# Kernel optimization log

Measured on AMD Instinct MI355X. Metric: run time of the kernel, lower is better.

Reference implementation:

```python
import jax, jax.numpy as jnp
import numpy as np

B, N, COUT, CIN, H, W = 16, 4, 256, 256, 64, 64


def setup_inputs() -> dict:
    key = jax.random.key(0)
    k1, k2, k3, k4 = jax.random.split(key, 4)
    x = jax.random.normal(k1, (B, CIN, H, W), jnp.float32)
    alphas = jax.random.uniform(k2, (B, N), jnp.float32)          # routing weights (lambdas)
    angles = jax.random.normal(k3, (B, N), jnp.float32) * 0.5     # thetas, mixed signs
    # kaiming_normal_(mode='fan_out', relu): std = sqrt(2 / (Cout * k * k))
    std = np.sqrt(2.0 / (COUT * 9)).astype(np.float32)
    weight = jax.random.normal(k4, (N, COUT, CIN, 3, 3), jnp.float32) * std
    return {"x": x, "alphas": alphas, "angles": angles, "weight": weight}


def _rot_mats(thetas):
    """thetas: [M] -> rotation matrices [M, 9, 9] (row, col), matching torch builder."""
    xc = jnp.cos(thetas)
    ys = jnp.sin(thetas)
    a = xc - ys
    b = xc * ys
    c = xc + ys
    z = jnp.zeros_like(xc)
    o = jnp.ones_like(xc)

    def mat(rows):
        # rows: list of 9 lists of 9 [M]-arrays -> [M, 9, 9]
        return jnp.stack([jnp.stack(r, axis=-1) for r in rows], axis=-2)

    pos = mat([
        [a, 1 - a, z, z, z, z, z, z, z],
        [z, xc - b, b, z, 1 - c + b, ys - b, z, z, z],
        [z, z, a, z, z, 1 - a, z, z, z],
        [b, ys - b, z, xc - b, 1 - c + b, z, z, z, z],
        [z, z, z, z, o, z, z, z, z],
        [z, z, z, z, 1 - c + b, xc - b, z, ys - b, b],
        [z, z, z, 1 - a, z, z, a, z, z],
        [z, z, z, ys - b, 1 - c + b, z, b, xc - b, z],
        [z, z, z, z, z, z, z, 1 - a, a],
    ])
    neg = mat([
        [c, z, z, 1 - c, z, z, z, z, z],
        [-b, xc + b, z, b - ys, 1 - a - b, z, z, z, z],
        [z, 1 - c, c, z, z, z, z, z, z],
        [z, z, z, xc + b, 1 - a - b, z, -b, b - ys, z],
        [z, z, z, z, o, z, z, z, z],
        [z, b - ys, -b, z, 1 - a - b, xc + b, z, z, z],
        [z, z, z, z, z, z, c, 1 - c, z],
        [z, z, z, z, 1 - a - b, b - ys, z, xc + b, -b],
        [z, z, z, z, z, 1 - c, z, z, c],
    ])
    m = (thetas >= 0).astype(thetas.dtype)[:, None, None]
    return m * pos + (1 - m) * neg


def reference(x, alphas, angles, weight):
    bsz, Cin, h, w = x.shape
    n, Cout = weight.shape[0], weight.shape[1]
    # [bsz, n, 9, 9] rotation matrices scaled by routing lambdas
    rm = _rot_mats(angles.reshape(-1)).reshape(bsz, n, 9, 9)
    rm = rm * alphas[:, :, None, None]
    # weights [n, Cout, Cin, 3, 3] -> [n, 9, Cout*Cin]
    Wf = weight.transpose(0, 3, 4, 1, 2).reshape(n, 9, Cout * Cin)
    # mix over kernel_number n and source tap q -> per-sample rotated kernels
    rw = jnp.einsum('bnpq,nqm->bpm', rm, Wf)          # [bsz, 9, Cout*Cin]
    rw = rw.reshape(bsz, 3, 3, Cout, Cin).transpose(0, 3, 4, 1, 2)
    rw = rw.reshape(bsz * Cout, Cin, 3, 3)
    # per-sample conv via grouped conv on flattened batch
    xr = x.reshape(1, bsz * Cin, h, w)
    out = jax.lax.conv_general_dilated(
        xr, rw, window_strides=(1, 1), padding=((1, 1), (1, 1)),
        dimension_numbers=('NCHW', 'OIHW', 'NCHW'), feature_group_count=bsz)
    return out.reshape(bsz, Cout, out.shape[2], out.shape[3])
```

## Files before the change

### kernel.cpp

```cpp
#include <hip/hip_runtime.h>
#include <hip/hip_bf16.h>

#define B_    16
#define N_    4
#define COUT  256
#define CIN   256
#define H_    64
#define W_    64
#define K_TOT (CIN * 9)
#define HW    (H_ * W_)
#define NKT   72
#define PAD   66
#define PLANE (PAD * PAD)

typedef __attribute__((ext_vector_type(8))) short short8;
typedef __attribute__((ext_vector_type(4))) float f32x4;
typedef unsigned short ushort_t;

static __device__ __forceinline__ ushort_t f2bf(float f) {
    __hip_bfloat16 h = __float2bfloat16(f);
    return *reinterpret_cast<ushort_t*>(&h);
}

typedef __attribute__((address_space(3))) unsigned int lds_u32;
typedef __attribute__((address_space(1))) const unsigned int glb_u32;
static __device__ __forceinline__ void gl_lds16(const ushort_t* g, ushort_t* l) {
    __builtin_amdgcn_global_load_lds((glb_u32*)g, (lds_u32*)l, 16, 0, 0);
}

#define BARRIER() asm volatile("s_barrier" ::: "memory")
#define VMCNTN(N) asm volatile("s_waitcnt vmcnt(" #N ")" ::: "memory")

__global__ void rot_mats_kernel(const float* __restrict__ alphas,
                                const float* __restrict__ angles,
                                float* __restrict__ rm) {
    int i = threadIdx.x;
    if (i >= B_ * N_) return;
    float th = angles[i], al = alphas[i];
    float xc = cosf(th), ys = sinf(th);
    float a = xc - ys, b = xc * ys, c = xc + ys;
    float r[81];
#pragma unroll
    for (int j = 0; j < 81; ++j) r[j] = 0.f;
    if (th >= 0.f) {
        r[0] = a;          r[1] = 1.f - a;
        r[10] = xc - b;    r[11] = b;        r[13] = 1.f - c + b; r[14] = ys - b;
        r[20] = a;         r[23] = 1.f - a;
        r[27] = b;         r[28] = ys - b;   r[30] = xc - b;      r[31] = 1.f - c + b;
        r[40] = 1.f;
        r[49] = 1.f - c + b; r[50] = xc - b; r[52] = ys - b;      r[53] = b;
        r[57] = 1.f - a;   r[60] = a;
        r[66] = ys - b;    r[67] = 1.f - c + b; r[69] = b;        r[70] = xc - b;
        r[79] = 1.f - a;   r[80] = a;
    } else {
        r[0] = c;          r[3] = 1.f - c;
        r[9] = -b;         r[10] = xc + b;   r[12] = b - ys;      r[13] = 1.f - a - b;
        r[19] = 1.f - c;   r[20] = c;
        r[30] = xc + b;    r[31] = 1.f - a - b; r[33] = -b;       r[34] = b - ys;
        r[40] = 1.f;
        r[46] = b - ys;    r[47] = -b;       r[49] = 1.f - a - b; r[50] = xc + b;
        r[60] = c;         r[61] = 1.f - c;
        r[67] = 1.f - a - b; r[68] = b - ys; r[70] = xc + b;      r[71] = -b;
        r[77] = 1.f - c;   r[80] = c;
    }
#pragma unroll
    for (int j = 0; j < 81; ++j) rm[i * 81 + j] = r[j] * al;
}

__global__ __launch_bounds__(256)
void build_rw_kernel(const float* __restrict__ weight,
                     const float* __restrict__ rm,
                     ushort_t* __restrict__ rw) {
    __shared__ float rms[N_ * 81];
    int tid = threadIdx.x;
    int b = blockIdx.y;
    for (int j = tid; j < N_ * 81; j += 256)
        rms[j] = rm[b * N_ * 81 + j];
    __syncthreads();

    int idx = blockIdx.x * 256 + tid;
    int cout = idx >> 8, cin = idx & 255;

    float wv[N_][9];
#pragma unroll
    for (int n = 0; n < N_; ++n)
#pragma unroll
        for (int q = 0; q < 9; ++q)
            wv[n][q] = weight[(size_t)(n * (COUT * CIN) + idx) * 9 + q];

    ushort_t* dst = rw + (size_t)(b * COUT + cout) * K_TOT + cin;
#pragma unroll
    for (int p = 0; p < 9; ++p) {
        float s = 0.f;
#pragma unroll
        for (int n = 0; n < N_; ++n)
#pragma unroll
            for (int q = 0; q < 9; ++q)
                s += rms[n * 81 + p * 9 + q] * wv[n][q];
        dst[p * 256] = f2bf(s);
    }
}

__global__ __launch_bounds__(256)
void halo_zero_kernel(ushort_t* __restrict__ xt) {
    ushort_t* base = xt + (size_t)blockIdx.x * PLANE * 64;
    int t = threadIdx.x;
    for (int i = t; i < 260; i += 256) {
        int py, px;
        if (i < 66)       { py = 0;  px = i; }
        else if (i < 132) { py = 65; px = i - 66; }
        else if (i < 196) { py = i - 132 + 1; px = 0; }
        else              { py = i - 196 + 1; px = 65; }
        ushort_t* d = base + (size_t)(py * PAD + px) * 64;
        int4 z = {0, 0, 0, 0};
#pragma unroll
        for (int q = 0; q < 8; ++q) *(int4*)(d + q * 8) = z;
    }
}

__global__ __launch_bounds__(256)
void nhwc_kernel(const float* __restrict__ x, ushort_t* __restrict__ xt) {
    int y    = blockIdx.x;
    int cb32 = blockIdx.y;
    int b    = blockIdx.z;
    __shared__ ushort_t tileT[64][40];
    int t = threadIdx.x;

    int ci = t & 31, seg = t >> 5;
    const float* src = x + ((size_t)(b * CIN + cb32 * 32 + ci) * HW + y * 64 + seg * 8);
    float4 f0 = ((const float4*)src)[0];
    float4 f1 = ((const float4*)src)[1];
#pragma unroll
    for (int q = 0; q < 4; ++q) tileT[seg * 8 + q][ci]     = f2bf(((float*)&f0)[q]);
#pragma unroll
    for (int q = 0; q < 4; ++q) tileT[seg * 8 + 4 + q][ci] = f2bf(((float*)&f1)[q]);
    __syncthreads();

    int px = t >> 2, cseg = t & 3;
    ushort_t* dst = xt + ((size_t)(b * 4 + (cb32 >> 1)) * PLANE + (y + 1) * PAD + px + 1) * 64
                       + (cb32 & 1) * 32 + cseg * 8;
    *(int4*)dst = *(const int4*)&tileT[px][cseg * 8];
}

__global__ __launch_bounds__(512, 4)
void conv_kernel(const ushort_t* __restrict__ xt,
                 const ushort_t* __restrict__ rw,
                 float* __restrict__ out) {
    int bid0 = blockIdx.x;
    int bid = (bid0 & 7) * 64 + (bid0 >> 3);
    int ch    = bid & 1;
    int ptile = (bid >> 1) & 15;
    int b     = bid >> 5;
    int m0 = ch * 128;
    int y0 = ptile * 4;
    int tid = threadIdx.x;
    int lane = tid & 63, wid = tid >> 6;
    int wm = wid >> 2, wn = wid & 3;
    int rA = lane & 15, kseg = lane >> 4;

    __shared__ __align__(16) ushort_t As[3][4096];
    __shared__ __align__(16) ushort_t Bs[3][8192];
    ushort_t* AsB = &As[0][0];
    ushort_t* BsB = &Bs[0][0];

    f32x4 acc[4][4] = {};

    const ushort_t* rwb = rw + (size_t)(b * COUT + m0) * K_TOT;
    const ushort_t* xtb = xt + ((size_t)b * 4 * PLANE + (size_t)y0 * PAD) * 64;

    {
    }
    int la = tid >> 3, sa = tid & 7;
    int ca = sa ^ (la & 7);
    const ushort_t* aSrc = rwb + (size_t)(2 * la + (ca >> 2)) * K_TOT + (ca & 3) * 8;
    const int aDst = tid * 8;
    int bsrc[2], bDst[2];
#pragma unroll
    for (int i = 0; i < 2; ++i) {
        int u = i * 512 + tid;
        int lb = u >> 3, sb = u & 7;
        int cb = sb ^ (lb & 7);
        int px = 2 * lb + (cb >> 2);
        bsrc[i] = ((px >> 6) * PAD + (px & 63)) * 64 + (cb & 3) * 8;
        bDst[i] = u * 8;
    }
    const int slotR = (kseg + 4 * (rA & 1)) ^ ((rA >> 1) & 7);
    const int aRd = (wm * 32 + (rA >> 1)) * 64 + slotR * 8;
    const int bRd = (wn * 32 + (rA >> 1)) * 64 + slotR * 8;

#define STAGE(KT, Q)                                                           \
    {                                                                          \
        int p_ = (KT) >> 3, sub_ = (KT) & 7;                                   \
        int ph_ = p_ / 3, pw_ = p_ - 3 * ph_;                                  \
        gl_lds16(aSrc + p_ * 256 + sub_ * 32, AsB + (Q) * 4096 + aDst);        \
        const ushort_t* sb_ = xtb + (size_t)((sub_ >> 1) * PLANE + ph_ * PAD + pw_) * 64 \
                              + (sub_ & 1) * 32;                               \
        gl_lds16(sb_ + bsrc[0], BsB + (Q) * 8192 + bDst[0]);                   \
        gl_lds16(sb_ + bsrc[1], BsB + (Q) * 8192 + bDst[1]);                   \
    }

    STAGE(0, 0);
    STAGE(1, 1);
    VMCNTN(3);
    BARRIER();

    int qc = 0;
    for (int kt = 0; kt < NKT; ++kt) {
        int qs = qc + 2; if (qs >= 3) qs -= 3;
        if (kt + 2 < NKT) STAGE(kt + 2, qs);

        short8 af[4], bf[4];
#pragma unroll
        for (int mi = 0; mi < 4; ++mi)
            af[mi] = *(const short8*)(AsB + qc * 4096 + aRd + mi * 512);
#pragma unroll
        for (int ni = 0; ni < 4; ++ni)
            bf[ni] = *(const short8*)(BsB + qc * 8192 + bRd + ni * 512);

        __builtin_amdgcn_s_setprio(1);
#pragma unroll
        for (int mi = 0; mi < 4; ++mi)
#pragma unroll
            for (int ni = 0; ni < 4; ++ni)
                acc[mi][ni] = __builtin_amdgcn_mfma_f32_16x16x32_bf16(
                    af[mi], bf[ni], acc[mi][ni], 0, 0, 0);
        __builtin_amdgcn_s_setprio(0);

        if (kt <= NKT - 3)      { VMCNTN(3); }
        else if (kt == NKT - 2) { VMCNTN(0); }
        BARRIER();
        qc = (qc == 2) ? 0 : qc + 1;
    }
#undef STAGE

    int row0 = (lane >> 4) * 4;
    int col  = lane & 15;
    float* outb = out + ((size_t)(b * COUT) + m0) * HW + ptile * 256;
#pragma unroll
    for (int mi = 0; mi < 4; ++mi)
#pragma unroll
        for (int ni = 0; ni < 4; ++ni)
#pragma unroll
            for (int rr = 0; rr < 4; ++rr) {
                int m = wm * 64 + mi * 16 + row0 + rr;
                int n = wn * 64 + ni * 16 + col;
                outb[(size_t)m * HW + n] = acc[mi][ni][rr];
            }
}

extern "C" void kernel_launch(void* const* d_in, const int* in_sizes, int n_in,
                              void* d_out, int out_size, void* d_ws, size_t ws_size,
                              hipStream_t stream) {
    const float* x      = (const float*)d_in[0];
    const float* alphas = (const float*)d_in[1];
    const float* angles = (const float*)d_in[2];
    const float* weight = (const float*)d_in[3];
    float* out = (float*)d_out;

    ushort_t* rw = (ushort_t*)d_ws;
    ushort_t* xt = (ushort_t*)((char*)d_ws + (size_t)B_ * COUT * K_TOT * 2);
    float*    rm = (float*)((char*)d_ws + (size_t)B_ * COUT * K_TOT * 2
                                        + (size_t)64 * PLANE * 64 * 2);

    rot_mats_kernel<<<1, 64, 0, stream>>>(alphas, angles, rm);
    build_rw_kernel<<<dim3(COUT * CIN / 256, B_), 256, 0, stream>>>(weight, rm, rw);
    halo_zero_kernel<<<64, 256, 0, stream>>>(xt);
    nhwc_kernel<<<dim3(64, 8, B_), 256, 0, stream>>>(x, xt);
    conv_kernel<<<512, 512, 0, stream>>>(xt, rw, out);
}
```

Before: 122.8 us.

## Enlarge conv tile to full 256 output channels with split MFMA phases

Each conv block now computes all 256 output channels for its pixel tile instead of 128. That halves the grid to 256 blocks and lets each block reuse its loaded input tile twice as much. The K-step is split into two MFMA halves, with the A and B global-to-LDS stages interleaved between barriers. Accumulators double to 32 f32x4 per thread and occupancy drops to 2 blocks/SM with more LDS. This risks register pressure, lower parallelism (256 blocks on 256 CUs), and extra barriers.

```diff
diff --git a/kernel.cpp b/kernel.cpp
--- a/kernel.cpp
+++ b/kernel.cpp
@@ -142,109 +142,120 @@
     *(int4*)dst = *(const int4*)&tileT[px][cseg * 8];
 }
 
-__global__ __launch_bounds__(512, 4)
+__global__ __launch_bounds__(512, 2)
 void conv_kernel(const ushort_t* __restrict__ xt,
                  const ushort_t* __restrict__ rw,
                  float* __restrict__ out) {
     int bid0 = blockIdx.x;
-    int bid = (bid0 & 7) * 64 + (bid0 >> 3);
-    int ch    = bid & 1;
-    int ptile = (bid >> 1) & 15;
-    int b     = bid >> 5;
-    int m0 = ch * 128;
+    int bid = (bid0 & 7) * 32 + (bid0 >> 3);
+    int b     = bid >> 4;
+    int ptile = bid & 15;
     int y0 = ptile * 4;
     int tid = threadIdx.x;
     int lane = tid & 63, wid = tid >> 6;
     int wm = wid >> 2, wn = wid & 3;
     int rA = lane & 15, kseg = lane >> 4;
 
-    __shared__ __align__(16) ushort_t As[3][4096];
+    __shared__ __align__(16) ushort_t As[3][8192];
     __shared__ __align__(16) ushort_t Bs[3][8192];
     ushort_t* AsB = &As[0][0];
     ushort_t* BsB = &Bs[0][0];
 
-    f32x4 acc[4][4] = {};
-
-    const ushort_t* rwb = rw + (size_t)(b * COUT + m0) * K_TOT;
+    f32x4 acc[8][4] = {};
+
+    const ushort_t* rwb = rw + (size_t)b * COUT * K_TOT;
     const ushort_t* xtb = xt + ((size_t)b * 4 * PLANE + (size_t)y0 * PAD) * 64;
 
-    {
-    }
-    int la = tid >> 3, sa = tid & 7;
-    int ca = sa ^ (la & 7);
-    const ushort_t* aSrc = rwb + (size_t)(2 * la + (ca >> 2)) * K_TOT + (ca & 3) * 8;
-    const int aDst = tid * 8;
-    int bsrc[2], bDst[2];
+    int asrc[2], bsrc[2], uDst[2];
 #pragma unroll
     for (int i = 0; i < 2; ++i) {
         int u = i * 512 + tid;
-        int lb = u >> 3, sb = u & 7;
-        int cb = sb ^ (lb & 7);
-        int px = 2 * lb + (cb >> 2);
-        bsrc[i] = ((px >> 6) * PAD + (px & 63)) * 64 + (cb & 3) * 8;
-        bDst[i] = u * 8;
+        int l = u >> 3, s = u & 7;
+        int c = s ^ (l & 7);
+        int row = 2 * l + (c >> 2);
+        asrc[i] = row * K_TOT + (c & 3) * 8;
+        bsrc[i] = ((row >> 6) * PAD + (row & 63)) * 64 + (c & 3) * 8;
+        uDst[i] = u * 8;
     }
     const int slotR = (kseg + 4 * (rA & 1)) ^ ((rA >> 1) & 7);
-    const int aRd = (wm * 32 + (rA >> 1)) * 64 + slotR * 8;
+    const int aRd = (wm * 64 + (rA >> 1)) * 64 + slotR * 8;
     const int bRd = (wn * 32 + (rA >> 1)) * 64 + slotR * 8;
 
-#define STAGE(KT, Q)                                                           \
+#define STAGE_A(KT, Q)                                                         \
+    {                                                                          \
+        int p_ = (KT) >> 3, sub_ = (KT) & 7;                                   \
+        int ako = p_ * 256 + sub_ * 32;                                        \
+        gl_lds16(rwb + asrc[0] + ako, AsB + (Q) * 8192 + uDst[0]);             \
+        gl_lds16(rwb + asrc[1] + ako, AsB + (Q) * 8192 + uDst[1]);             \
+    }
+
+#define STAGE_B(KT, Q)                                                         \
     {                                                                          \
         int p_ = (KT) >> 3, sub_ = (KT) & 7;                                   \
         int ph_ = p_ / 3, pw_ = p_ - 3 * ph_;                                  \
-        gl_lds16(aSrc + p_ * 256 + sub_ * 32, AsB + (Q) * 4096 + aDst);        \
         const ushort_t* sb_ = xtb + (size_t)((sub_ >> 1) * PLANE + ph_ * PAD + pw_) * 64 \
                               + (sub_ & 1) * 32;                               \
-        gl_lds16(sb_ + bsrc[0], BsB + (Q) * 8192 + bDst[0]);                   \
-        gl_lds16(sb_ + bsrc[1], BsB + (Q) * 8192 + bDst[1]);                   \
-    }
-
-    STAGE(0, 0);
-    STAGE(1, 1);
-    VMCNTN(3);
+        gl_lds16(sb_ + bsrc[0], BsB + (Q) * 8192 + uDst[0]);                   \
+        gl_lds16(sb_ + bsrc[1], BsB + (Q) * 8192 + uDst[1]);                   \
+    }
+
+#define DO_MFMA(MH)                                                            \
+    __builtin_amdgcn_s_setprio(1);                                             \
+    _Pragma("unroll")                                                          \
+    for (int mi = 0; mi < 4; ++mi)                                             \
+        _Pragma("unroll")                                                      \
+        for (int ni = 0; ni < 4; ++ni)                                         \
+            acc[(MH) * 4 + mi][ni] = __builtin_amdgcn_mfma_f32_16x16x32_bf16(  \
+                af[mi], bf[ni], acc[(MH) * 4 + mi][ni], 0, 0, 0);              \
+    __builtin_amdgcn_s_setprio(0);
+
+    STAGE_A(0, 0); STAGE_B(0, 0);
+    STAGE_A(1, 1); STAGE_B(1, 1);
+    VMCNTN(4);
     BARRIER();
 
+    short8 af[4], bf[4];
     int qc = 0;
     for (int kt = 0; kt < NKT; ++kt) {
         int qs = qc + 2; if (qs >= 3) qs -= 3;
-        if (kt + 2 < NKT) STAGE(kt + 2, qs);
-
-        short8 af[4], bf[4];
+        bool more = (kt + 2 < NKT);
 #pragma unroll
         for (int mi = 0; mi < 4; ++mi)
-            af[mi] = *(const short8*)(AsB + qc * 4096 + aRd + mi * 512);
+            af[mi] = *(const short8*)(AsB + qc * 8192 + aRd + mi * 512);
 #pragma unroll
         for (int ni = 0; ni < 4; ++ni)
             bf[ni] = *(const short8*)(BsB + qc * 8192 + bRd + ni * 512);
-
-        __builtin_amdgcn_s_setprio(1);
+        if (more) STAGE_A(kt + 2, qs);
+        BARRIER();
+        DO_MFMA(0);
+        BARRIER();
 #pragma unroll
         for (int mi = 0; mi < 4; ++mi)
-#pragma unroll
-            for (int ni = 0; ni < 4; ++ni)
-                acc[mi][ni] = __builtin_amdgcn_mfma_f32_16x16x32_bf16(
-                    af[mi], bf[ni], acc[mi][ni], 0, 0, 0);
-        __builtin_amdgcn_s_setprio(0);
-
-        if (kt <= NKT - 3)      { VMCNTN(3); }
+            af[mi] = *(const short8*)(AsB + qc * 8192 + aRd + (mi + 4) * 512);
+        if (more) STAGE_B(kt + 2, qs);
+        BARRIER();
+        DO_MFMA(1);
+        if (kt <= NKT - 3)      { VMCNTN(4); }
         else if (kt == NKT - 2) { VMCNTN(0); }
         BARRIER();
         qc = (qc == 2) ? 0 : qc + 1;
     }
-#undef STAGE
+#undef STAGE_A
+#undef STAGE_B
+#undef DO_MFMA
 
     int row0 = (lane >> 4) * 4;
     int col  = lane & 15;
-    float* outb = out + ((size_t)(b * COUT) + m0) * HW + ptile * 256;
-#pragma unroll
-    for (int mi = 0; mi < 4; ++mi)
-#pragma unroll
-        for (int ni = 0; ni < 4; ++ni)
+    float* outb = out + (size_t)b * COUT * HW + ptile * 256;
+#pragma unroll
+    for (int am = 0; am < 8; ++am)
+#pragma unroll
+        for (int an = 0; an < 4; ++an)
 #pragma unroll
             for (int rr = 0; rr < 4; ++rr) {
-                int m = wm * 64 + mi * 16 + row0 + rr;
-                int n = wn * 64 + ni * 16 + col;
-                outb[(size_t)m * HW + n] = acc[mi][ni][rr];
+                int m = wm * 128 + am * 16 + row0 + rr;
+                int n = wn * 64 + an * 16 + col;
+                outb[(size_t)m * HW + n] = acc[am][an][rr];
             }
 }
 
@@ -266,5 +277,5 @@
     build_rw_kernel<<<dim3(COUT * CIN / 256, B_), 256, 0, stream>>>(weight, rm, rw);
     halo_zero_kernel<<<64, 256, 0, stream>>>(xt);
     nhwc_kernel<<<dim3(64, 8, B_), 256, 0, stream>>>(x, xt);
-    conv_kernel<<<512, 512, 0, stream>>>(xt, rw, out);
-}
+    conv_kernel<<<256, 512, 0, stream>>>(xt, rw, out);
+}
```

Result: no change. 121.5 us (-1.0%).
